# Kernel tuning notes

Measured on AMD Instinct MI355X. Metric: run time of the kernel, lower is better.

The kernel has to match this reference:

```python
import jax, jax.numpy as jnp
import numpy as np

N_NODES = 50000
N_EDGES = 800000
N_GRAPHS = 128
D_IN, D_HID, D_OUT = 128, 128, 128  # gnn_input_dim, gnn_hidden_dim, gnn_output_dim
EPS = 1e-5
NEG_SLOPE = 0.01


def setup_inputs() -> dict:
    key = jax.random.key(0)
    ks = jax.random.split(key, 16)
    x = jax.random.normal(ks[0], (N_NODES, D_IN), jnp.float32)
    edge_index = jax.random.randint(ks[1], (2, N_EDGES), 0, N_NODES, dtype=jnp.int64)
    batch = jnp.sort(jax.random.randint(ks[2], (N_NODES,), 0, N_GRAPHS, dtype=jnp.int64))

    def lin(k, fi, fo):
        return jax.random.normal(k, (fi, fo), jnp.float32) * (1.0 / np.sqrt(fi))

    d2, d4 = 2 * D_HID, 4 * D_HID
    return {
        "x": x, "edge_index": edge_index, "batch": batch, "batch_size": N_GRAPHS,
        "W1": lin(ks[3], D_IN, d2), "b1": jnp.zeros((d2,), jnp.float32),
        "g1": jnp.ones((d2,), jnp.float32), "be1": jnp.zeros((d2,), jnp.float32),
        "W2": lin(ks[4], d2, d4), "b2": jnp.zeros((d4,), jnp.float32),
        "g2": jnp.ones((d4,), jnp.float32), "be2": jnp.zeros((d4,), jnp.float32),
        "W3": lin(ks[5], d4, d4), "b3": jnp.zeros((d4,), jnp.float32),
        "g3": jnp.ones((d4,), jnp.float32), "be3": jnp.zeros((d4,), jnp.float32),
        "Wf": lin(ks[6], d4, D_OUT), "bf": jnp.zeros((D_OUT,), jnp.float32),
    }


def _layernorm(h, g, b):
    mu = jnp.mean(h, axis=-1, keepdims=True)
    var = jnp.mean(jnp.square(h - mu), axis=-1, keepdims=True)
    return (h - mu) * jax.lax.rsqrt(var + EPS) * g + b


def _gcn_conv(h, W, b, src, dst, norm, n):
    # h' = D^-1/2 (A+I) D^-1/2 (h W) + b   (PyG GCNConv with self-loops)
    m = h @ W                                    # [N, F_out]
    msg = m[src] * norm[:, None]                 # [E+N, F_out]
    return jax.ops.segment_sum(msg, dst, num_segments=n) + b


def reference(x, edge_index, batch, batch_size, W1, b1, g1, be1,
              W2, b2, g2, be2, W3, b3, g3, be3, Wf, bf):
    n = x.shape[0]
    loop = jnp.arange(n, dtype=edge_index.dtype)
    src = jnp.concatenate([edge_index[0], loop])
    dst = jnp.concatenate([edge_index[1], loop])
    deg = jax.ops.segment_sum(jnp.ones_like(dst, dtype=x.dtype), dst, num_segments=n)
    dinv = jax.lax.rsqrt(deg)                    # deg >= 1 due to self loops
    norm = dinv[src] * dinv[dst]

    h = _gcn_conv(x, W1, b1, src, dst, norm, n)
    h = jax.nn.leaky_relu(_layernorm(h, g1, be1), NEG_SLOPE)
    h = _gcn_conv(h, W2, b2, src, dst, norm, n)
    h = jax.nn.leaky_relu(_layernorm(h, g2, be2), NEG_SLOPE)
    h = _gcn_conv(h, W3, b3, src, dst, norm, n)
    h = _layernorm(h, g3, be3)

    # global average pool per graph
    sums = jax.ops.segment_sum(h, batch, num_segments=batch_size)
    cnt = jax.ops.segment_sum(jnp.ones((n,), h.dtype), batch, num_segments=batch_size)
    pooled = sums / jnp.maximum(cnt, 1.0)[:, None]
    return pooled @ Wf + bf
```

## Files before the change

### kernel.cpp

```cpp
#include <hip/hip_runtime.h>
#include <hip/hip_bf16.h>
#include <math.h>

#define GRAPHS 128
#define SCAN_B 256
#define BM 128
#define BN 128
#define BK 64
#define PCH 128

typedef __attribute__((ext_vector_type(8))) short bfrag8;
typedef __attribute__((ext_vector_type(4))) float f32x4;

__device__ inline unsigned short f2b(float f) {
    unsigned int u = __float_as_uint(f);
    unsigned int r = (u + 0x7fffu + ((u >> 16) & 1u)) >> 16;
    return (unsigned short)r;
}
__device__ inline float b2f(unsigned short u) {
    return __uint_as_float(((unsigned int)u) << 16);
}
__device__ inline void unpack8(float* v, uint4 u) {
    v[0] = b2f(u.x & 0xffffu); v[1] = b2f(u.x >> 16);
    v[2] = b2f(u.y & 0xffffu); v[3] = b2f(u.y >> 16);
    v[4] = b2f(u.z & 0xffffu); v[5] = b2f(u.z >> 16);
    v[6] = b2f(u.w & 0xffffu); v[7] = b2f(u.w >> 16);
}

__device__ inline void gload16(const void* g, void* l) {
    typedef unsigned int __attribute__((address_space(1))) gu32;
    typedef unsigned int __attribute__((address_space(3))) su32;
    __builtin_amdgcn_global_load_lds((const gu32*)g, (su32*)l, 16, 0, 0);
}

__device__ inline int xcd_vid(int p, int nwg) {
    int q = nwg >> 3, r = nwg & 7, x = p & 7, ix = p >> 3;
    return (x < r ? x * (q + 1) : r * (q + 1) + (x - r) * q) + ix;
}


__global__ void k_count(const int* __restrict__ dst, int* __restrict__ cnt, int E) {
    int i = blockIdx.x * blockDim.x + threadIdx.x;
    if (i < E) atomicAdd(&cnt[dst[i]], 1);
}

__global__ void k_scan1(const int* __restrict__ cnt, int* __restrict__ excl,
                        int* __restrict__ bsum, int n) {
    __shared__ int sh[SCAN_B];
    int t = threadIdx.x;
    int i = blockIdx.x * SCAN_B + t;
    int v = (i < n) ? cnt[i] : 0;
    sh[t] = v;
    __syncthreads();
    for (int off = 1; off < SCAN_B; off <<= 1) {
        int x = (t >= off) ? sh[t - off] : 0;
        __syncthreads();
        sh[t] += x;
        __syncthreads();
    }
    if (i < n) excl[i] = sh[t] - v;
    if (t == SCAN_B - 1) bsum[blockIdx.x] = sh[t];
}

__global__ void k_scan2(int* __restrict__ bsum, int nb) {
    __shared__ int sh[SCAN_B];
    int t = threadIdx.x;
    int v = (t < nb) ? bsum[t] : 0;
    sh[t] = v;
    __syncthreads();
    for (int off = 1; off < SCAN_B; off <<= 1) {
        int x = (t >= off) ? sh[t - off] : 0;
        __syncthreads();
        sh[t] += x;
        __syncthreads();
    }
    if (t < nb) bsum[t] = sh[t] - v;
}

__global__ void k_scan3(int* __restrict__ rowstart, const int* __restrict__ bsum,
                        const int* __restrict__ cnt, float* __restrict__ dinv,
                        int* __restrict__ cursor, int n, int E) {
    int i = blockIdx.x * SCAN_B + threadIdx.x;
    if (i < n) {
        rowstart[i] += bsum[blockIdx.x];
        cursor[i] = 0;
        dinv[i] = rsqrtf((float)cnt[i] + 1.0f);
    }
    if (i == 0) rowstart[n] = E;
}

__global__ void k_scatter_csr(const int* __restrict__ src, const int* __restrict__ dst,
                              const float* __restrict__ dinv, const int* __restrict__ rowstart,
                              int* __restrict__ cursor, int2* __restrict__ csr, int E) {
    int e = blockIdx.x * blockDim.x + threadIdx.x;
    if (e >= E) return;
    int s = src[e], d = dst[e];
    int pos = rowstart[d] + atomicAdd(&cursor[d], 1);
    int2 c;
    c.x = s;
    c.y = __float_as_int(dinv[s] * dinv[d]);
    csr[pos] = c;
}


__global__ void k_wt3(const float* __restrict__ W1, const float* __restrict__ W2,
                      const float* __restrict__ W3, unsigned short* __restrict__ T1,
                      unsigned short* __restrict__ T2, unsigned short* __restrict__ T3) {
    int idx = blockIdx.x * 256 + threadIdx.x;
    const float* W; unsigned short* T; int K, N;
    if (idx < 32768) { W = W1; T = T1; K = 128; N = 256; }
    else if (idx < 163840) { idx -= 32768; W = W2; T = T2; K = 256; N = 512; }
    else { idx -= 163840; if (idx >= 262144) return; W = W3; T = T3; K = 512; N = 512; }
    int k = idx / N, n2 = idx - k * N;
    T[(size_t)n2 * K + k] = f2b(W[idx]);
}


__global__ void k_x2q(const float* __restrict__ x, signed char* __restrict__ q,
                      float* __restrict__ sc, int n, int mpad) {
    int row = blockIdx.x * 4 + (threadIdx.x >> 6);
    int lane = threadIdx.x & 63;
    if (row >= mpad) return;
    signed char* qp = q + (size_t)row * 128 + lane * 2;
    if (row >= n) {
        *(unsigned short*)qp = 0;
        if (lane == 0) sc[row] = 0.f;
        return;
    }
    float2 v = *(const float2*)(x + (size_t)row * 128 + lane * 2);
    float mx = fmaxf(fabsf(v.x), fabsf(v.y));
#pragma unroll
    for (int m = 1; m < 64; m <<= 1) mx = fmaxf(mx, __shfl_xor(mx, m));
    float inv = (mx > 0.f) ? 127.0f / mx : 0.f;
    int q0 = __float2int_rn(v.x * inv), q1 = __float2int_rn(v.y * inv);
    *(unsigned short*)qp = (unsigned short)((q0 & 0xff) | ((q1 & 0xff) << 8));
    if (lane == 0) sc[row] = mx * (1.0f / 127.0f);
}


__device__ inline void acc8i(float* a, uint2 u, float w) {
    a[0] += (float)(signed char)(u.x) * w;
    a[1] += (float)(signed char)(u.x >> 8) * w;
    a[2] += (float)(signed char)(u.x >> 16) * w;
    a[3] += (float)(signed char)(u.x >> 24) * w;
    a[4] += (float)(signed char)(u.y) * w;
    a[5] += (float)(signed char)(u.y >> 8) * w;
    a[6] += (float)(signed char)(u.y >> 16) * w;
    a[7] += (float)(signed char)(u.y >> 24) * w;
}

template <int F>
__global__ void k_agg8(const signed char* __restrict__ q8, const float* __restrict__ scale,
                       unsigned short* __restrict__ agg, const int* __restrict__ rowstart,
                       const int2* __restrict__ csr, const float* __restrict__ dinv,
                       int n, int mpad) {
    constexpr int TPN = F / 8;
    constexpr int NPB = 256 / TPN;
    int node = blockIdx.x * NPB + (int)(threadIdx.x / TPN);
    int fo = (int)(threadIdx.x % TPN) * 8;
    if (node >= mpad) return;
    uint4* dst = (uint4*)(agg + (size_t)node * F + fo);
    if (node >= n) { uint4 z = {0u, 0u, 0u, 0u}; *dst = z; return; }

    const signed char* qf = q8 + fo;
    float di = dinv[node];
    float a[8] = {};
    {
        uint2 u = *(const uint2*)(qf + (size_t)node * F);
        acc8i(a, u, di * di * scale[node]);
    }
    int b = rowstart[node], e = rowstart[node + 1];
    int j = b;
    for (; j + 2 <= e; j += 2) {
        int2 c0 = csr[j], c1 = csr[j + 1];
        uint2 u0 = *(const uint2*)(qf + (size_t)c0.x * F);
        uint2 u1 = *(const uint2*)(qf + (size_t)c1.x * F);
        float w0 = __int_as_float(c0.y) * scale[c0.x];
        float w1 = __int_as_float(c1.y) * scale[c1.x];
        acc8i(a, u0, w0);
        acc8i(a, u1, w1);
    }
    for (; j < e; ++j) {
        int2 c = csr[j];
        uint2 u = *(const uint2*)(qf + (size_t)c.x * F);
        acc8i(a, u, __int_as_float(c.y) * scale[c.x]);
    }
    uint4 o;
    o.x = (unsigned)f2b(a[0]) | ((unsigned)f2b(a[1]) << 16);
    o.y = (unsigned)f2b(a[2]) | ((unsigned)f2b(a[3]) << 16);
    o.z = (unsigned)f2b(a[4]) | ((unsigned)f2b(a[5]) << 16);
    o.w = (unsigned)f2b(a[6]) | ((unsigned)f2b(a[7]) << 16);
    *dst = o;
}


__global__ __launch_bounds__(256) void k_gemm_bf16(
    const unsigned short* __restrict__ A, const unsigned short* __restrict__ BT,
    const float* __restrict__ bias, unsigned short* __restrict__ C,
    int K, int N, int ncb) {
    __shared__ __align__(16) char sA[BM * BK * 2];
    __shared__ __align__(16) char sB[BN * BK * 2];

    const int vid = xcd_vid((int)blockIdx.x, (int)gridDim.x);
    const int rb = vid / ncb;
    const int cb = vid - rb * ncb;
    const int tid = threadIdx.x;
    const int lane = tid & 63;
    const int wave = tid >> 6;
    const int wr = wave >> 1, wc = wave & 1;
    const size_t row0 = (size_t)rb * BM;
    const size_t col0 = (size_t)cb * BN;

    const unsigned short* srcA[4];
    const unsigned short* srcB[4];
    char* dstA[4];
    char* dstB[4];
#pragma unroll
    for (int c = 0; c < 4; ++c) {
        int idx = c * 256 + tid;
        int row = idx >> 3;
        int cbl = ((idx & 7) << 4) ^ ((row & 7) << 4);
        srcA[c] = A + (row0 + row) * K + (cbl >> 1);
        srcB[c] = BT + (col0 + row) * K + (cbl >> 1);
        dstA[c] = sA + idx * 16;
        dstB[c] = sB + idx * 16;
    }

    const int fr = lane & 15;
    const int fg = lane >> 4;
    const int fsw = (lane & 7) << 4;
    int offA[4][2], offB[4][2];
#pragma unroll
    for (int t = 0; t < 4; ++t)
#pragma unroll
        for (int kk = 0; kk < 2; ++kk) {
            offA[t][kk] = (wr * 64 + t * 16 + fr) * (BK * 2) + ((kk * 64 + fg * 16) ^ fsw);
            offB[t][kk] = (wc * 64 + t * 16 + fr) * (BK * 2) + ((kk * 64 + fg * 16) ^ fsw);
        }

    f32x4 acc[4][4] = {};

    for (int k0 = 0; k0 < K; k0 += BK) {
#pragma unroll
        for (int c = 0; c < 4; ++c) gload16(srcA[c] + k0, dstA[c]);
#pragma unroll
        for (int c = 0; c < 4; ++c) gload16(srcB[c] + k0, dstB[c]);
        __syncthreads();
#pragma unroll
        for (int kk = 0; kk < 2; ++kk) {
            bfrag8 av[4], bv[4];
#pragma unroll
            for (int t = 0; t < 4; ++t) av[t] = *(const bfrag8*)(sA + offA[t][kk]);
#pragma unroll
            for (int t = 0; t < 4; ++t) bv[t] = *(const bfrag8*)(sB + offB[t][kk]);
#pragma unroll
            for (int i = 0; i < 4; ++i)
#pragma unroll
                for (int j = 0; j < 4; ++j)
                    acc[i][j] = __builtin_amdgcn_mfma_f32_16x16x32_bf16(av[i], bv[j],
                                                                        acc[i][j], 0, 0, 0);
        }
        __syncthreads();
    }

#pragma unroll
    for (int i = 0; i < 4; ++i) {
#pragma unroll
        for (int j = 0; j < 4; ++j) {
            size_t r = row0 + wr * 64 + i * 16 + fg * 4;
            size_t cc = col0 + wc * 64 + j * 16 + fr;
            float bb = bias[cc];
#pragma unroll
            for (int q = 0; q < 4; ++q)
                C[(r + q) * N + cc] = f2b(acc[i][j][q] + bb);
        }
    }
}


template <int F, bool LRELU>
__global__ void k_lnr8(const unsigned short* __restrict__ z, signed char* __restrict__ q8,
                       float* __restrict__ scale, const float* __restrict__ g,
                       const float* __restrict__ be, int mpad) {
    constexpr int V = F / 64;
    int row = blockIdx.x * 4 + (threadIdx.x >> 6);
    int lane = threadIdx.x & 63;
    const unsigned short* p = z + (size_t)row * F + lane * V;
    float v[V];
    if constexpr (V == 8) {
        uint4 u = *(const uint4*)p;
        unpack8(v, u);
    } else {
        uint2 u = *(const uint2*)p;
        v[0] = b2f(u.x & 0xffffu); v[1] = b2f(u.x >> 16);
        v[2] = b2f(u.y & 0xffffu); v[3] = b2f(u.y >> 16);
    }
    float s = 0.f, q = 0.f;
#pragma unroll
    for (int k = 0; k < V; ++k) { s += v[k]; q += v[k] * v[k]; }
#pragma unroll
    for (int m = 1; m < 64; m <<= 1) {
        s += __shfl_xor(s, m);
        q += __shfl_xor(q, m);
    }
    float mu = s * (1.0f / F);
    float var = q * (1.0f / F) - mu * mu;
    float rs = rsqrtf(var + 1e-5f);

    float y[V];
    float mx = 0.f;
#pragma unroll
    for (int k = 0; k < V; ++k) {
        float yy = (v[k] - mu) * rs * g[lane * V + k] + be[lane * V + k];
        if (LRELU) yy = fmaxf(yy, 0.f) + 0.01f * fminf(yy, 0.f);
        y[k] = yy;
        mx = fmaxf(mx, fabsf(yy));
    }
#pragma unroll
    for (int m = 1; m < 64; m <<= 1) mx = fmaxf(mx, __shfl_xor(mx, m));

    float inv = (mx > 0.f) ? 127.0f / mx : 0.f;
    unsigned int ob[V / 4];
#pragma unroll
    for (int k = 0; k < V; k += 4) {
        int q0 = __float2int_rn(y[k] * inv);
        int q1 = __float2int_rn(y[k + 1] * inv);
        int q2 = __float2int_rn(y[k + 2] * inv);
        int q3 = __float2int_rn(y[k + 3] * inv);
        ob[k / 4] = (q0 & 0xff) | ((q1 & 0xff) << 8) | ((q2 & 0xff) << 16) | ((q3 & 0xff) << 24);
    }
    signed char* qp = q8 + (size_t)row * F + lane * V;
    if constexpr (V == 8) *(uint2*)qp = *(uint2*)ob;
    else                  *(unsigned int*)qp = ob[0];
    if (lane == 0) scale[row] = mx * (1.0f / 127.0f);
}


__global__ void k_pool4(const unsigned short* __restrict__ z, const float* __restrict__ g,
                        const float* __restrict__ be, const int* __restrict__ batch,
                        float* __restrict__ pooled, int n) {
    int i0 = blockIdx.x * PCH;
    int iend = i0 + PCH; if (iend > n) iend = n;
    int w = threadIdx.x >> 6, lane = threadIdx.x & 63;
    int f0 = lane * 8;
    float gk[8], ek[8];
    {
        float4 ga = *(const float4*)(g + f0), gb = *(const float4*)(g + f0 + 4);
        float4 ea = *(const float4*)(be + f0), eb = *(const float4*)(be + f0 + 4);
        gk[0] = ga.x; gk[1] = ga.y; gk[2] = ga.z; gk[3] = ga.w;
        gk[4] = gb.x; gk[5] = gb.y; gk[6] = gb.z; gk[7] = gb.w;
        ek[0] = ea.x; ek[1] = ea.y; ek[2] = ea.z; ek[3] = ea.w;
        ek[4] = eb.x; ek[5] = eb.y; ek[6] = eb.z; ek[7] = eb.w;
    }
    float a[8] = {};
    int cur = -1;
    for (int i = i0 + w; i < iend; i += 4) {
        int gg = batch[i];
        if (gg != cur) {
            if (cur >= 0) {
                float* pp = pooled + (size_t)cur * 512 + f0;
#pragma unroll
                for (int k = 0; k < 8; ++k) atomicAdd(&pp[k], a[k]);
            }
#pragma unroll
            for (int k = 0; k < 8; ++k) a[k] = 0.f;
            cur = gg;
        }
        uint4 u = *(const uint4*)(z + (size_t)i * 512 + f0);
        float v[8]; unpack8(v, u);
        float s = 0.f, q = 0.f;
#pragma unroll
        for (int k = 0; k < 8; ++k) { s += v[k]; q += v[k] * v[k]; }
#pragma unroll
        for (int m = 1; m < 64; m <<= 1) {
            s += __shfl_xor(s, m);
            q += __shfl_xor(q, m);
        }
        float mu = s * (1.0f / 512.0f);
        float var = q * (1.0f / 512.0f) - mu * mu;
        float rs = rsqrtf(var + 1e-5f);
#pragma unroll
        for (int k = 0; k < 8; ++k) a[k] += (v[k] - mu) * rs * gk[k] + ek[k];
    }
    if (cur >= 0) {
        float* pp = pooled + (size_t)cur * 512 + f0;
#pragma unroll
        for (int k = 0; k < 8; ++k) atomicAdd(&pp[k], a[k]);
    }
}


__global__ void k_final(const float* __restrict__ pooled, const int* __restrict__ batch,
                        const float* __restrict__ Wf, const float* __restrict__ bf,
                        float* __restrict__ out, int n) {
    int gph = blockIdx.x;
    int o = threadIdx.x;
    int lo = 0, hi = n;
    while (lo < hi) { int mid = (lo + hi) >> 1; if (batch[mid] < gph) lo = mid + 1; else hi = mid; }
    int start = lo;
    lo = start; hi = n;
    while (lo < hi) { int mid = (lo + hi) >> 1; if (batch[mid] < gph + 1) lo = mid + 1; else hi = mid; }
    int end = lo;
    float inv = 1.0f / fmaxf((float)(end - start), 1.0f);

    __shared__ float p[512];
    for (int k = threadIdx.x; k < 512; k += 128) p[k] = pooled[(size_t)gph * 512 + k] * inv;
    __syncthreads();
    float acc = bf[o];
#pragma unroll 8
    for (int k = 0; k < 512; ++k) acc += p[k] * Wf[(size_t)k * 128 + o];
    out[(size_t)gph * 128 + o] = acc;
}


static inline size_t align_up(size_t x) { return (x + 255) & ~(size_t)255; }

extern "C" void kernel_launch(void* const* d_in, const int* in_sizes, int n_in,
                              void* d_out, int out_size, void* d_ws, size_t ws_size,
                              hipStream_t stream) {
    const float* x     = (const float*)d_in[0];
    const int*   ei    = (const int*)d_in[1];
    const int*   batch = (const int*)d_in[2];
    const float* W1 = (const float*)d_in[4],  *b1 = (const float*)d_in[5];
    const float* g1 = (const float*)d_in[6],  *be1= (const float*)d_in[7];
    const float* W2 = (const float*)d_in[8],  *b2 = (const float*)d_in[9];
    const float* g2 = (const float*)d_in[10], *be2= (const float*)d_in[11];
    const float* W3 = (const float*)d_in[12], *b3 = (const float*)d_in[13];
    const float* g3 = (const float*)d_in[14], *be3= (const float*)d_in[15];
    const float* Wf = (const float*)d_in[16], *bf = (const float*)d_in[17];
    float* out = (float*)d_out;

    const int N = in_sizes[0] / 128;
    const int E = in_sizes[1] / 2;
    const int Mpad = ((N + BM - 1) / BM) * BM;
    const int* src = ei;
    const int* dst = ei + E;

    char* ws = (char*)d_ws;
    size_t off = 0;
    auto take = [&](size_t bytes) { char* p = ws + off; off += align_up(bytes); return p; };

    unsigned short* zb      = (unsigned short*)take((size_t)Mpad * 512 * 2);
    unsigned short* aggb    = (unsigned short*)take((size_t)Mpad * 512 * 2);
    signed char*    q8      = (signed char*)take((size_t)Mpad * 512);
    float*          scale   = (float*)take((size_t)Mpad * 4);
    signed char*    q8x     = (signed char*)take((size_t)Mpad * 128);
    float*          sx      = (float*)take((size_t)Mpad * 4);
    unsigned short* wt1     = (unsigned short*)take((size_t)256 * 128 * 2);
    unsigned short* wt2     = (unsigned short*)take((size_t)512 * 256 * 2);
    unsigned short* wt3     = (unsigned short*)take((size_t)512 * 512 * 2);
    float*          dinv    = (float*)take((size_t)N * 4);
    int*            rowstart= (int*)  take((size_t)(N + 1) * 4);
    int*            cnt     = (int*)  take((size_t)N * 4);
    int*            cursor  = (int*)  take((size_t)N * 4);
    int*            bsum    = (int*)  take((size_t)SCAN_B * 4);
    int2*           csr     = (int2*) take((size_t)E * 8);
    float*          pooled  = (float*)take((size_t)GRAPHS * 512 * 4);

    const int nb = (N + SCAN_B - 1) / SCAN_B;
    const int NR4 = Mpad / 4;

    hipMemsetAsync(cnt, 0, (size_t)N * 4, stream);
    k_count<<<(E + 255) / 256, 256, 0, stream>>>(dst, cnt, E);
    k_scan1<<<nb, SCAN_B, 0, stream>>>(cnt, rowstart, bsum, N);
    k_scan2<<<1, SCAN_B, 0, stream>>>(bsum, nb);
    k_scan3<<<nb, SCAN_B, 0, stream>>>(rowstart, bsum, cnt, dinv, cursor, N, E);
    k_scatter_csr<<<(E + 255) / 256, 256, 0, stream>>>(src, dst, dinv, rowstart, cursor, csr, E);

    k_wt3<<<(425984 + 255) / 256, 256, 0, stream>>>(W1, W2, W3, wt1, wt2, wt3);

    k_x2q<<<NR4, 256, 0, stream>>>(x, q8x, sx, N, Mpad);

    k_agg8<128><<<Mpad / 16, 256, 0, stream>>>(q8x, sx, aggb, rowstart, csr, dinv, N, Mpad);
    k_gemm_bf16<<<(Mpad / BM) * 2, 256, 0, stream>>>(aggb, wt1, b1, zb, 128, 256, 2);
    k_lnr8<256, true><<<NR4, 256, 0, stream>>>(zb, q8, scale, g1, be1, Mpad);

    k_agg8<256><<<Mpad / 8, 256, 0, stream>>>(q8, scale, aggb, rowstart, csr, dinv, N, Mpad);
    k_gemm_bf16<<<(Mpad / BM) * 4, 256, 0, stream>>>(aggb, wt2, b2, zb, 256, 512, 4);
    k_lnr8<512, true><<<NR4, 256, 0, stream>>>(zb, q8, scale, g2, be2, Mpad);

    k_agg8<512><<<Mpad / 4, 256, 0, stream>>>(q8, scale, aggb, rowstart, csr, dinv, N, Mpad);
    k_gemm_bf16<<<(Mpad / BM) * 4, 256, 0, stream>>>(aggb, wt3, b3, zb, 512, 512, 4);

    hipMemsetAsync(pooled, 0, (size_t)GRAPHS * 512 * 4, stream);
    k_pool4<<<(N + PCH - 1) / PCH, 256, 0, stream>>>(zb, g3, be3, batch, pooled, N);
    k_final<<<GRAPHS, 128, 0, stream>>>(pooled, batch, Wf, bf, out, N);
}
```

Before: 437.1 us.

## Quantize aggregated features and weights to int8 and use int8 MFMA GEMMs

The aggregation kernels now emit per-row int8-quantized outputs with a scale instead of bf16, and the weights are quantized per output column to int8. The three GEMMs switch from bf16 MFMA to i32 16x16x64 int8 MFMA, applying row and column scales in the epilogue. This halves GEMM operand traffic and the aggregation write bandwidth, and doubles the MFMA K-throughput per instruction. The cost is lower accuracy from a second int8 quantization stage applied to both activations and weights.

```diff
diff --git a/kernel.cpp b/kernel.cpp
--- a/kernel.cpp
+++ b/kernel.cpp
@@ -6,11 +6,9 @@
 #define SCAN_B 256
 #define BM 128
 #define BN 128
-#define BK 64
 #define PCH 128
 
-typedef __attribute__((ext_vector_type(8))) short bfrag8;
-typedef __attribute__((ext_vector_type(4))) float f32x4;
+typedef __attribute__((ext_vector_type(4))) int i32x4;
 
 __device__ inline unsigned short f2b(float f) {
     unsigned int u = __float_as_uint(f);
@@ -103,16 +101,31 @@
 }
 
 
-__global__ void k_wt3(const float* __restrict__ W1, const float* __restrict__ W2,
-                      const float* __restrict__ W3, unsigned short* __restrict__ T1,
-                      unsigned short* __restrict__ T2, unsigned short* __restrict__ T3) {
-    int idx = blockIdx.x * 256 + threadIdx.x;
-    const float* W; unsigned short* T; int K, N;
-    if (idx < 32768) { W = W1; T = T1; K = 128; N = 256; }
-    else if (idx < 163840) { idx -= 32768; W = W2; T = T2; K = 256; N = 512; }
-    else { idx -= 163840; if (idx >= 262144) return; W = W3; T = T3; K = 512; N = 512; }
-    int k = idx / N, n2 = idx - k * N;
-    T[(size_t)n2 * K + k] = f2b(W[idx]);
+__global__ void k_wtq(const float* __restrict__ W1, const float* __restrict__ W2,
+                      const float* __restrict__ W3, signed char* __restrict__ T1,
+                      signed char* __restrict__ T2, signed char* __restrict__ T3,
+                      float* __restrict__ S1, float* __restrict__ S2,
+                      float* __restrict__ S3) {
+    int w = blockIdx.x * 4 + (threadIdx.x >> 6);
+    int lane = threadIdx.x & 63;
+    const float* W; signed char* T; float* S; int K, N, col;
+    if (w < 256) { W = W1; T = T1; S = S1; K = 128; N = 256; col = w; }
+    else if (w < 768) { W = W2; T = T2; S = S2; K = 256; N = 512; col = w - 256; }
+    else { W = W3; T = T3; S = S3; K = 512; N = 512; col = w - 768; }
+    int epl = K >> 6;
+    float v[8];
+    float mx = 0.f;
+    for (int j = 0; j < epl; ++j) {
+        float x = W[(size_t)(lane * epl + j) * N + col];
+        v[j] = x;
+        mx = fmaxf(mx, fabsf(x));
+    }
+#pragma unroll
+    for (int m = 1; m < 64; m <<= 1) mx = fmaxf(mx, __shfl_xor(mx, m));
+    float inv = (mx > 0.f) ? 127.0f / mx : 0.f;
+    signed char* tp = T + (size_t)col * K + lane * epl;
+    for (int j = 0; j < epl; ++j) tp[j] = (signed char)__float2int_rn(v[j] * inv);
+    if (lane == 0) S[col] = mx * (1.0f / 127.0f);
 }
 
 
@@ -151,16 +164,21 @@
 
 template <int F>
 __global__ void k_agg8(const signed char* __restrict__ q8, const float* __restrict__ scale,
-                       unsigned short* __restrict__ agg, const int* __restrict__ rowstart,
-                       const int2* __restrict__ csr, const float* __restrict__ dinv,
-                       int n, int mpad) {
+                       signed char* __restrict__ qa, float* __restrict__ sa,
+                       const int* __restrict__ rowstart, const int2* __restrict__ csr,
+                       const float* __restrict__ dinv, int n, int mpad) {
     constexpr int TPN = F / 8;
     constexpr int NPB = 256 / TPN;
     int node = blockIdx.x * NPB + (int)(threadIdx.x / TPN);
-    int fo = (int)(threadIdx.x % TPN) * 8;
+    int sub = (int)(threadIdx.x % TPN);
+    int fo = sub * 8;
     if (node >= mpad) return;
-    uint4* dst = (uint4*)(agg + (size_t)node * F + fo);
-    if (node >= n) { uint4 z = {0u, 0u, 0u, 0u}; *dst = z; return; }
+    signed char* outp = qa + (size_t)node * F + fo;
+    if (node >= n) {
+        *(uint2*)outp = uint2{0u, 0u};
+        if (sub == 0) sa[node] = 0.f;
+        return;
+    }
 
     const signed char* qf = q8 + fo;
     float di = dinv[node];
@@ -185,21 +203,30 @@
         uint2 u = *(const uint2*)(qf + (size_t)c.x * F);
         acc8i(a, u, __int_as_float(c.y) * scale[c.x]);
     }
-    uint4 o;
-    o.x = (unsigned)f2b(a[0]) | ((unsigned)f2b(a[1]) << 16);
-    o.y = (unsigned)f2b(a[2]) | ((unsigned)f2b(a[3]) << 16);
-    o.z = (unsigned)f2b(a[4]) | ((unsigned)f2b(a[5]) << 16);
-    o.w = (unsigned)f2b(a[6]) | ((unsigned)f2b(a[7]) << 16);
-    *dst = o;
-}
-
-
-__global__ __launch_bounds__(256) void k_gemm_bf16(
-    const unsigned short* __restrict__ A, const unsigned short* __restrict__ BT,
+    float mx = 0.f;
+#pragma unroll
+    for (int k = 0; k < 8; ++k) mx = fmaxf(mx, fabsf(a[k]));
+#pragma unroll
+    for (int m = 1; m < TPN; m <<= 1) mx = fmaxf(mx, __shfl_xor(mx, m));
+    float inv = (mx > 0.f) ? 127.0f / mx : 0.f;
+    unsigned int o0 = 0, o1 = 0;
+#pragma unroll
+    for (int k = 0; k < 4; ++k) {
+        o0 |= ((unsigned)(__float2int_rn(a[k] * inv) & 0xff)) << (8 * k);
+        o1 |= ((unsigned)(__float2int_rn(a[k + 4] * inv) & 0xff)) << (8 * k);
+    }
+    *(uint2*)outp = uint2{o0, o1};
+    if (sub == 0) sa[node] = mx * (1.0f / 127.0f);
+}
+
+
+__global__ __launch_bounds__(256) void k_gemm_i8(
+    const signed char* __restrict__ A, const float* __restrict__ srow,
+    const signed char* __restrict__ BT, const float* __restrict__ scol,
     const float* __restrict__ bias, unsigned short* __restrict__ C,
     int K, int N, int ncb) {
-    __shared__ __align__(16) char sA[BM * BK * 2];
-    __shared__ __align__(16) char sB[BN * BK * 2];
+    __shared__ __align__(16) char sA[BM * 128];
+    __shared__ __align__(16) char sB[BN * 128];
 
     const int vid = xcd_vid((int)blockIdx.x, (int)gridDim.x);
     const int rb = vid / ncb;
@@ -211,8 +238,8 @@
     const size_t row0 = (size_t)rb * BM;
     const size_t col0 = (size_t)cb * BN;
 
-    const unsigned short* srcA[4];
-    const unsigned short* srcB[4];
+    const signed char* srcA[4];
+    const signed char* srcB[4];
     char* dstA[4];
     char* dstB[4];
 #pragma unroll
@@ -220,8 +247,8 @@
         int idx = c * 256 + tid;
         int row = idx >> 3;
         int cbl = ((idx & 7) << 4) ^ ((row & 7) << 4);
-        srcA[c] = A + (row0 + row) * K + (cbl >> 1);
-        srcB[c] = BT + (col0 + row) * K + (cbl >> 1);
+        srcA[c] = A + (row0 + row) * K + cbl;
+        srcB[c] = BT + (col0 + row) * K + cbl;
         dstA[c] = sA + idx * 16;
         dstB[c] = sB + idx * 16;
     }
@@ -234,13 +261,13 @@
     for (int t = 0; t < 4; ++t)
 #pragma unroll
         for (int kk = 0; kk < 2; ++kk) {
-            offA[t][kk] = (wr * 64 + t * 16 + fr) * (BK * 2) + ((kk * 64 + fg * 16) ^ fsw);
-            offB[t][kk] = (wc * 64 + t * 16 + fr) * (BK * 2) + ((kk * 64 + fg * 16) ^ fsw);
+            offA[t][kk] = (wr * 64 + t * 16 + fr) * 128 + ((kk * 64 + fg * 16) ^ fsw);
+            offB[t][kk] = (wc * 64 + t * 16 + fr) * 128 + ((kk * 64 + fg * 16) ^ fsw);
         }
 
-    f32x4 acc[4][4] = {};
-
-    for (int k0 = 0; k0 < K; k0 += BK) {
+    i32x4 acc[4][4] = {};
+
+    for (int k0 = 0; k0 < K; k0 += 128) {
 #pragma unroll
         for (int c = 0; c < 4; ++c) gload16(srcA[c] + k0, dstA[c]);
 #pragma unroll
@@ -248,20 +275,27 @@
         __syncthreads();
 #pragma unroll
         for (int kk = 0; kk < 2; ++kk) {
-            bfrag8 av[4], bv[4];
-#pragma unroll
-            for (int t = 0; t < 4; ++t) av[t] = *(const bfrag8*)(sA + offA[t][kk]);
-#pragma unroll
-            for (int t = 0; t < 4; ++t) bv[t] = *(const bfrag8*)(sB + offB[t][kk]);
+            i32x4 av[4], bv[4];
+#pragma unroll
+            for (int t = 0; t < 4; ++t) av[t] = *(const i32x4*)(sA + offA[t][kk]);
+#pragma unroll
+            for (int t = 0; t < 4; ++t) bv[t] = *(const i32x4*)(sB + offB[t][kk]);
 #pragma unroll
             for (int i = 0; i < 4; ++i)
 #pragma unroll
                 for (int j = 0; j < 4; ++j)
-                    acc[i][j] = __builtin_amdgcn_mfma_f32_16x16x32_bf16(av[i], bv[j],
-                                                                        acc[i][j], 0, 0, 0);
+                    acc[i][j] = __builtin_amdgcn_mfma_i32_16x16x64_i8(av[i], bv[j],
+                                                                      acc[i][j], 0, 0, 0);
         }
         __syncthreads();
     }
+
+    float sr[4][4];
+#pragma unroll
+    for (int i = 0; i < 4; ++i)
+#pragma unroll
+        for (int q = 0; q < 4; ++q)
+            sr[i][q] = srow[row0 + wr * 64 + i * 16 + fg * 4 + q];
 
 #pragma unroll
     for (int i = 0; i < 4; ++i) {
@@ -269,10 +303,11 @@
         for (int j = 0; j < 4; ++j) {
             size_t r = row0 + wr * 64 + i * 16 + fg * 4;
             size_t cc = col0 + wc * 64 + j * 16 + fr;
+            float scc = scol[cc];
             float bb = bias[cc];
 #pragma unroll
             for (int q = 0; q < 4; ++q)
-                C[(r + q) * N + cc] = f2b(acc[i][j][q] + bb);
+                C[(r + q) * N + cc] = f2b((float)acc[i][j][q] * (sr[i][q] * scc) + bb);
         }
     }
 }
@@ -441,14 +476,18 @@
     auto take = [&](size_t bytes) { char* p = ws + off; off += align_up(bytes); return p; };
 
     unsigned short* zb      = (unsigned short*)take((size_t)Mpad * 512 * 2);
-    unsigned short* aggb    = (unsigned short*)take((size_t)Mpad * 512 * 2);
+    signed char*    qa      = (signed char*)take((size_t)Mpad * 512);
+    float*          sa      = (float*)take((size_t)Mpad * 4);
     signed char*    q8      = (signed char*)take((size_t)Mpad * 512);
     float*          scale   = (float*)take((size_t)Mpad * 4);
     signed char*    q8x     = (signed char*)take((size_t)Mpad * 128);
     float*          sx      = (float*)take((size_t)Mpad * 4);
-    unsigned short* wt1     = (unsigned short*)take((size_t)256 * 128 * 2);
-    unsigned short* wt2     = (unsigned short*)take((size_t)512 * 256 * 2);
-    unsigned short* wt3     = (unsigned short*)take((size_t)512 * 512 * 2);
+    signed char*    wq1     = (signed char*)take((size_t)256 * 128);
+    signed char*    wq2     = (signed char*)take((size_t)512 * 256);
+    signed char*    wq3     = (signed char*)take((size_t)512 * 512);
+    float*          sc1     = (float*)take(256 * 4);
+    float*          sc2     = (float*)take(512 * 4);
+    float*          sc3     = (float*)take(512 * 4);
     float*          dinv    = (float*)take((size_t)N * 4);
     int*            rowstart= (int*)  take((size_t)(N + 1) * 4);
     int*            cnt     = (int*)  take((size_t)N * 4);
@@ -467,20 +506,20 @@
     k_scan3<<<nb, SCAN_B, 0, stream>>>(rowstart, bsum, cnt, dinv, cursor, N, E);
     k_scatter_csr<<<(E + 255) / 256, 256, 0, stream>>>(src, dst, dinv, rowstart, cursor, csr, E);
 
-    k_wt3<<<(425984 + 255) / 256, 256, 0, stream>>>(W1, W2, W3, wt1, wt2, wt3);
+    k_wtq<<<320, 256, 0, stream>>>(W1, W2, W3, wq1, wq2, wq3, sc1, sc2, sc3);
 
     k_x2q<<<NR4, 256, 0, stream>>>(x, q8x, sx, N, Mpad);
 
-    k_agg8<128><<<Mpad / 16, 256, 0, stream>>>(q8x, sx, aggb, rowstart, csr, dinv, N, Mpad);
-    k_gemm_bf16<<<(Mpad / BM) * 2, 256, 0, stream>>>(aggb, wt1, b1, zb, 128, 256, 2);
+    k_agg8<128><<<Mpad / 16, 256, 0, stream>>>(q8x, sx, qa, sa, rowstart, csr, dinv, N, Mpad);
+    k_gemm_i8<<<(Mpad / BM) * 2, 256, 0, stream>>>(qa, sa, wq1, sc1, b1, zb, 128, 256, 2);
     k_lnr8<256, true><<<NR4, 256, 0, stream>>>(zb, q8, scale, g1, be1, Mpad);
 
-    k_agg8<256><<<Mpad / 8, 256, 0, stream>>>(q8, scale, aggb, rowstart, csr, dinv, N, Mpad);
-    k_gemm_bf16<<<(Mpad / BM) * 4, 256, 0, stream>>>(aggb, wt2, b2, zb, 256, 512, 4);
+    k_agg8<256><<<Mpad / 8, 256, 0, stream>>>(q8, scale, qa, sa, rowstart, csr, dinv, N, Mpad);
+    k_gemm_i8<<<(Mpad / BM) * 4, 256, 0, stream>>>(qa, sa, wq2, sc2, b2, zb, 256, 512, 4);
     k_lnr8<512, true><<<NR4, 256, 0, stream>>>(zb, q8, scale, g2, be2, Mpad);
 
-    k_agg8<512><<<Mpad / 4, 256, 0, stream>>>(q8, scale, aggb, rowstart, csr, dinv, N, Mpad);
-    k_gemm_bf16<<<(Mpad / BM) * 4, 256, 0, stream>>>(aggb, wt3, b3, zb, 512, 512, 4);
+    k_agg8<512><<<Mpad / 4, 256, 0, stream>>>(q8, scale, qa, sa, rowstart, csr, dinv, N, Mpad);
+    k_gemm_i8<<<(Mpad / BM) * 4, 256, 0, stream>>>(qa, sa, wq3, sc3, b3, zb, 512, 512, 4);
 
     hipMemsetAsync(pooled, 0, (size_t)GRAPHS * 512 * 4, stream);
     k_pool4<<<(N + PCH - 1) / PCH, 256, 0, stream>>>(zb, g3, be3, batch, pooled, N);
```

Result: faster. 412.1 us (-5.7%).
